# Performance work log

Measured on AMD Instinct MI355X. Metric: run time of the kernel, lower is better.

Reference implementation:

```python
import math
import jax, jax.numpy as jnp
import numpy as np

K = 1.0            # Lorentz manifold curvature k
B, S = 4, 2048     # batch, seq_len
IN, H, OUT = 512, 8, 64   # in_channels, num_heads, out_channels (space dim; head_dim = OUT+1)


def setup_inputs() -> dict:
    key = jax.random.key(0)
    ks = jax.random.split(key, 8)
    std = 1.0 / math.sqrt(IN)
    return {
        "query_input": jax.random.normal(ks[0], (B, S, IN), jnp.float32),
        "source_input": jax.random.normal(ks[1], (B, S, IN), jnp.float32),
        # per-head HypLinear weights stacked on a leading head axis: [H, OUT, IN]
        "Wq_w": jax.random.normal(ks[2], (H, OUT, IN), jnp.float32) * std,
        "Wq_b": jnp.zeros((H, OUT), jnp.float32),
        "Wk_w": jax.random.normal(ks[3], (H, OUT, IN), jnp.float32) * std,
        "Wk_b": jnp.zeros((H, OUT), jnp.float32),
        "Wv_w": jax.random.normal(ks[4], (H, OUT, IN), jnp.float32) * std,
        "Wv_b": jnp.zeros((H, OUT), jnp.float32),
        "scale": jnp.array([math.sqrt(OUT)], jnp.float32),  # nn.Parameter([sqrt(out_channels)])
        "bias": jnp.zeros((), jnp.float32),                 # nn.Parameter(zeros(()))
    }


def hyp_linear(x, w, b):
    # HypLinear: linear map to space part, recompute Lorentz time coord sqrt(||x_s||^2 + k)
    sp = jnp.einsum('bsi,hoi->bsho', x, w) + b            # [B,S,H,OUT]
    t = jnp.sqrt(jnp.sum(sp * sp, axis=-1, keepdims=True) + K)
    return jnp.concatenate([t, sp], axis=-1)              # [B,S,H,OUT+1]


def reference(query_input, source_input, Wq_w, Wq_b, Wk_w, Wk_b, Wv_w, Wv_b, scale, bias):
    q = hyp_linear(query_input, Wq_w, Wq_b)   # [B,S,H,D], D = OUT+1
    k = hyp_linear(source_input, Wk_w, Wk_b)
    v = hyp_linear(source_input, Wv_w, Wv_b)

    # Lorentzian cinner: <x,y>_L = -x0*y0 + <x_s, y_s>
    sgn = jnp.concatenate([-jnp.ones((1,), q.dtype), jnp.ones((OUT,), q.dtype)])
    att = jnp.einsum('bqhd,bkhd->bhqk', q * sgn, k)       # [B,H,S,S]
    att = (2.0 + 2.0 * att) / scale[0] + bias

    causal = jnp.triu(jnp.full((S, S), -1e9, q.dtype), 1)  # causal mask (additive)
    att = jax.nn.softmax(att + causal, axis=-1)

    ctx = jnp.einsum('bhqk,bkhd->bqhd', att, v)           # [B,S,H,D]

    # manifold.mid_point over the heads axis (dim=-2)
    ave = jnp.mean(ctx, axis=2)                           # [B,S,D]
    inner = -ave[..., :1] ** 2 + jnp.sum(ave[..., 1:] ** 2, axis=-1, keepdims=True)
    denom = jnp.sqrt(jnp.maximum(jnp.abs(-inner), 1e-8))
    return math.sqrt(K) * ave / denom                     # [B,S,D]
```

## Files before the change

kernel.cpp:

```cpp
#include <hip/hip_runtime.h>

#define BATCH 4
#define SEQ   2048
#define INC   512
#define NH    8
#define OUTC  64
#define DD    65
#define NROW  (BATCH * NH * SEQ)

typedef float f32x4 __attribute__((ext_vector_type(4)));
typedef short short8 __attribute__((ext_vector_type(8)));
typedef short short4v __attribute__((ext_vector_type(4)));
typedef unsigned int uint2v __attribute__((ext_vector_type(2)));
typedef unsigned short us;

static __device__ __forceinline__ us f2b(float f) {
  unsigned int u = __float_as_uint(f);
  u = (u + 0x7FFFu + ((u >> 16) & 1u)) >> 16;
  return (us)u;
}
static __device__ __forceinline__ float b2f(us h) {
  return __uint_as_float(((unsigned int)h) << 16);
}
static __device__ __forceinline__ unsigned int pk2(float lo, float hi) {
  unsigned int r;
  asm("v_cvt_pk_bf16_f32 %0, %1, %2" : "=v"(r) : "v"(lo), "v"(hi));
  return r;
}

#define GLDS(g, l) __builtin_amdgcn_global_load_lds( \
    (const __attribute__((address_space(1))) void*)(g), \
    (__attribute__((address_space(3))) void*)(l), 16, 0, 0)

__global__ __launch_bounds__(256) void tobf16_kernel(
    const float* __restrict__ Xq, const float* __restrict__ Xs,
    const float* __restrict__ Wq, const float* __restrict__ Wk,
    const float* __restrict__ Wv,
    us* __restrict__ dXq, us* __restrict__ dXs,
    us* __restrict__ dWq, us* __restrict__ dWk, us* __restrict__ dWv)
{
  const int which = blockIdx.y;
  const float* src;
  us* dst;
  int n;
  switch (which) {
    case 0: src = Xq; dst = dXq; n = BATCH * SEQ * INC; break;
    case 1: src = Xs; dst = dXs; n = BATCH * SEQ * INC; break;
    case 2: src = Wq; dst = dWq; n = NH * OUTC * INC; break;
    case 3: src = Wk; dst = dWk; n = NH * OUTC * INC; break;
    default: src = Wv; dst = dWv; n = NH * OUTC * INC; break;
  }
  for (long i = (long)blockIdx.x * 256 + threadIdx.x; i * 4 < n;
       i += (long)gridDim.x * 256) {
    f32x4 v = *(const f32x4*)(src + i * 4);
    short4v o;
    o[0] = (short)f2b(v[0]); o[1] = (short)f2b(v[1]);
    o[2] = (short)f2b(v[2]); o[3] = (short)f2b(v[3]);
    *(short4v*)(dst + i * 4) = o;
  }
}

__global__ __launch_bounds__(256) void proj_kernel(
    const us* __restrict__ Xqb, const us* __restrict__ Xsb,
    const us* __restrict__ Wqb, const us* __restrict__ Wkb, const us* __restrict__ Wvb,
    const float* __restrict__ Bq, const float* __restrict__ Bk, const float* __restrict__ Bv,
    us* __restrict__ qs, float* __restrict__ qt,
    us* __restrict__ ks, unsigned int* __restrict__ kta,
    us* __restrict__ vs, us* __restrict__ vtc)
{
  const int which = blockIdx.z;
  const us* X = (which == 0) ? Xqb : Xsb;
  const us* W = (which == 0) ? Wqb : (which == 1 ? Wkb : Wvb);
  const float* Bb = (which == 0) ? Bq : (which == 1 ? Bk : Bv);
  us* outs = (which == 0) ? qs : (which == 1 ? ks : vs);

  const int lin = blockIdx.x;
  const int h   = (lin >> 3) & 7;
  const int m0  = (((lin >> 6) << 3) | (lin & 7)) * 64;
  const int n0  = h * 64;

  __shared__ alignas(16) us lX[2][64 * 64];
  __shared__ alignas(16) us lW[2][64 * 64];

  const int tid  = threadIdx.x;
  const int lane = tid & 63;
  const int wave = tid >> 6;
  const int arow = lane & 15;
  const int agrp = lane >> 4;
  const int rl   = lane >> 3;
  const int chx  = ((lane & 7) ^ rl) * 8;
  const int r0   = wave * 8 + rl;
  const int r1   = r0 + 32;

#define PSTAGE(buf, k0) do { \
    GLDS(X + (size_t)(m0 + r0) * INC + (k0) + chx, &lX[buf][wave * 512]); \
    GLDS(X + (size_t)(m0 + r1) * INC + (k0) + chx, &lX[buf][2048 + wave * 512]); \
    GLDS(W + (size_t)(n0 + r0) * INC + (k0) + chx, &lW[buf][wave * 512]); \
    GLDS(W + (size_t)(n0 + r1) * INC + (k0) + chx, &lW[buf][2048 + wave * 512]); \
  } while (0)

  f32x4 acc[4] = {};
  PSTAGE(0, 0);

  for (int kk = 0; kk < 8; ++kk) {
    const int cur = kk & 1;
    if (kk < 7) {
      PSTAGE(cur ^ 1, (kk + 1) * 64);
      asm volatile("s_waitcnt vmcnt(4)");
    } else {
      asm volatile("s_waitcnt vmcnt(0)");
    }
    __builtin_amdgcn_s_barrier();
#pragma unroll
    for (int kc = 0; kc < 2; ++kc) {
      short8 af = *(const short8*)&lX[cur][(wave * 16 + arow) * 64 + (((kc * 4 + agrp) ^ (arow & 7)) * 8)];
#pragma unroll
      for (int c = 0; c < 4; ++c) {
        short8 bf = *(const short8*)&lW[cur][(c * 16 + arow) * 64 + (((kc * 4 + agrp) ^ (arow & 7)) * 8)];
        acc[c] = __builtin_amdgcn_mfma_f32_16x16x32_bf16(af, bf, acc[c], 0, 0, 0);
      }
    }
    __builtin_amdgcn_s_barrier();
  }

  float bcol[4];
#pragma unroll
  for (int c = 0; c < 4; ++c) bcol[c] = Bb[n0 + c * 16 + arow];
#pragma unroll
  for (int r = 0; r < 4; ++r) {
    float s2 = 0.f;
#pragma unroll
    for (int c = 0; c < 4; ++c) {
      float v = acc[c][r] + bcol[c];
      acc[c][r] = v;
      s2 += v * v;
    }
    s2 += __shfl_xor(s2, 1); s2 += __shfl_xor(s2, 2);
    s2 += __shfl_xor(s2, 4); s2 += __shfl_xor(s2, 8);
    float tv = sqrtf(s2 + 1.0f);
    int gs = m0 + wave * 16 + agrp * 4 + r;
    int bi = gs >> 11, si = gs & (SEQ - 1);
    size_t rowbase = (size_t)(bi * NH + h) * SEQ + si;
    size_t obase = rowbase * 64;
#pragma unroll
    for (int c = 0; c < 4; ++c) outs[obase + c * 16 + arow] = f2b(acc[c][r]);
    if (arow == 0) {
      if (which == 0) {
        qt[rowbase] = tv;
      } else {
        us th = f2b(tv);
        us tl = f2b(tv - b2f(th));
        if (which == 1) {
          kta[rowbase] = (unsigned int)(us)(th ^ 0x8000)
                       | ((unsigned int)(us)(tl ^ 0x8000) << 16);
        } else {
          vtc[rowbase] = th;
          vtc[NROW + rowbase] = tl;
        }
      }
    }
  }
}

__global__ __launch_bounds__(256) void transpose_v_kernel(
    const us* __restrict__ vs, us* __restrict__ vT)
{
  const int bh = blockIdx.y;
  const int s0 = blockIdx.x * 64;
  __shared__ us lT[64 * 80];
  const int tid = threadIdx.x;
#pragma unroll
  for (int u0 = 0; u0 < 2; ++u0) {
    int u = tid + u0 * 256;
    int row = u >> 3, ch = u & 7;
    short8 v = *(const short8*)&vs[((size_t)bh * SEQ + s0 + row) * 64 + ch * 8];
    *(short8*)&lT[row * 80 + ch * 8] = v;
  }
  __syncthreads();
#pragma unroll
  for (int u0 = 0; u0 < 2; ++u0) {
    int u = tid + u0 * 256;
    int o = u >> 3, sc = u & 7;
    short8 w;
#pragma unroll
    for (int j = 0; j < 8; ++j) w[j] = lT[(sc * 8 + j) * 80 + o];
    *(short8*)&vT[((size_t)bh * 64 + o) * SEQ + s0 + sc * 8] = w;
  }
}

__global__ __launch_bounds__(256, 4) void attn_kernel(
    const us* __restrict__ qs, const float* __restrict__ qt,
    const us* __restrict__ ks, const unsigned int* __restrict__ kta,
    const us* __restrict__ vT, const us* __restrict__ vtc,
    const float* __restrict__ scale_p, float* __restrict__ part)
{
  const int f = blockIdx.x;
  const int xcd = f & 7, idx = f >> 3;
  const int bh = xcd * 4 + (idx >> 5);
  const int inner = idx & 31;
  const int xb = inner >> 1;
  const int hf = inner & 1;
  const float al2 = (2.0f / scale_p[0]) * 1.44269504088896f;

  __shared__ alignas(16) us lK[2][64 * 64];
  __shared__ alignas(16) us lV[2][64 * 64];
  __shared__ alignas(16) us lP[4][16 * 40];

  const int tid  = threadIdx.x;
  const int lane = tid & 63;
  const int wave = tid >> 6;
  const int arow = lane & 15;
  const int agrp = lane >> 4;

  const size_t bhbase = (size_t)bh * SEQ;
  const us* kgp = ks + bhbase * 64;
  const us* vgp = vT + (size_t)bh * 64 * SEQ;
  const unsigned int* ktp = kta + bhbase;
  const us* vtp = vtc + (size_t)(arow & 1) * NROW + bhbase;

  const int rl   = lane >> 3;
  const int chx  = ((lane & 7) ^ rl) * 8;
  const int r0s  = wave * 8 + rl;
  const int r1s  = r0s + 32;
  const int dsl0 = (agrp ^ (arow & 7)) * 8;
  const int dsl1 = ((4 + agrp) ^ (arow & 7)) * 8;
  us* myP = &lP[wave][0];
  const int pw0 = arow * 40 + agrp * 4;
  const int prd = arow * 40 + agrp * 8;

#define ASTAGE(buf, t64) do { \
    const int kk0 = (t64) * 64; \
    GLDS(kgp + (size_t)(kk0 + r0s) * 64 + chx, &lK[buf][wave * 512]); \
    GLDS(kgp + (size_t)(kk0 + r1s) * 64 + chx, &lK[buf][2048 + wave * 512]); \
    GLDS(vgp + (size_t)r0s * SEQ + kk0 + chx, &lV[buf][wave * 512]); \
    GLDS(vgp + (size_t)r1s * SEQ + kk0 + chx, &lV[buf][2048 + wave * 512]); \
  } while (0)

  short8 ones8, zero8 = {};
#pragma unroll
  for (int j = 0; j < 8; ++j) ones8[j] = (short)0x3F80;

  for (int seg = 0; seg < 2; ++seg) {
    const int qb = seg ? (31 - xb) : xb;
    const int q0 = qb * 64;
    const int c0 = (qb + 2) >> 1;
    const int t_lo = hf ? c0 : 0;
    const int t_hi = hf ? (qb + 1) : c0;
    const int nt = t_hi - t_lo;
    const int wq = wave * 16 + arow;

    f32x4 acc[5] = {};

    if (nt > 0) {
      const us* qp = qs + (bhbase + q0 + wq) * 64;
      short8 qf0 = *(const short8*)(qp + agrp * 8);
      short8 qf1 = *(const short8*)(qp + 32 + agrp * 8);
      float qtv = qt[bhbase + q0 + wq];
      us qh = f2b(qtv);
      us ql = f2b(qtv - b2f(qh));
      short8 qf2 = {};
      if (agrp == 0) { qf2[0] = (short)qh; qf2[1] = (short)qh; qf2[2] = (short)ql; }

      unsigned int ka[4];
      short8 va0, va1;
      {
        const int kk0 = t_lo * 64;
#pragma unroll
        for (int c = 0; c < 4; ++c) ka[c] = ktp[kk0 + c * 16 + arow];
        va0 = *(const short8*)(vtp + kk0 + agrp * 8);
        va1 = *(const short8*)(vtp + kk0 + 32 + agrp * 8);
      }
      __builtin_amdgcn_sched_barrier(0);
      ASTAGE(0, t_lo);
      __builtin_amdgcn_sched_barrier(0);

      for (int it = 0; it < nt; ++it) {
        const int t = t_lo + it;
        const int cur = it & 1;
        if (it < nt - 1) {
          ASTAGE(cur ^ 1, t + 1);
          __builtin_amdgcn_sched_barrier(0);
          if (it == 0) asm volatile("s_waitcnt vmcnt(4)");
          else         asm volatile("s_waitcnt vmcnt(10)");
        } else {
          __builtin_amdgcn_sched_barrier(0);
          if (nt > 1) asm volatile("s_waitcnt vmcnt(6)");
          else        asm volatile("s_waitcnt vmcnt(0)");
        }
        __builtin_amdgcn_sched_barrier(0);
        __builtin_amdgcn_s_barrier();

        const us* Kb = lK[cur];
        const us* Vb = lV[cur];

        f32x4 sS[4] = {};
        __builtin_amdgcn_s_setprio(1);
#pragma unroll
        for (int c = 0; c < 4; ++c) {
          short8 kf = *(const short8*)&Kb[(c * 16 + arow) * 64 + dsl0];
          sS[c] = __builtin_amdgcn_mfma_f32_16x16x32_bf16(kf, qf0, sS[c], 0, 0, 0);
        }
#pragma unroll
        for (int c = 0; c < 4; ++c) {
          short8 kf = *(const short8*)&Kb[(c * 16 + arow) * 64 + dsl1];
          sS[c] = __builtin_amdgcn_mfma_f32_16x16x32_bf16(kf, qf1, sS[c], 0, 0, 0);
        }
#pragma unroll
        for (int c = 0; c < 4; ++c) {
          short8 kf2 = {};
          if (agrp == 0) {
            unsigned int w0 = ka[c];
            kf2[0] = (short)(w0 & 0xFFFFu);
            kf2[1] = (short)(w0 >> 16);
            kf2[2] = (short)(w0 & 0xFFFFu);
          }
          sS[c] = __builtin_amdgcn_mfma_f32_16x16x32_bf16(kf2, qf2, sS[c], 0, 0, 0);
        }
        __builtin_amdgcn_s_setprio(0);

#pragma unroll
        for (int c = 0; c < 4; ++c)
#pragma unroll
          for (int r = 0; r < 4; ++r)
            sS[c][r] = exp2f(al2 * sS[c][r]);
        if (t == qb) {
#pragma unroll
          for (int c = 0; c < 4; ++c)
#pragma unroll
            for (int r = 0; r < 4; ++r)
              if (c * 16 + agrp * 4 + r > wq) sS[c][r] = 0.f;
        }

        {
          uint2v w;
          w[0] = pk2(sS[0][0], sS[0][1]); w[1] = pk2(sS[0][2], sS[0][3]);
          *(uint2v*)&myP[pw0] = w;
          w[0] = pk2(sS[1][0], sS[1][1]); w[1] = pk2(sS[1][2], sS[1][3]);
          *(uint2v*)&myP[pw0 + 16] = w;
          short8 pf = *(const short8*)&myP[prd];
          __builtin_amdgcn_s_setprio(1);
#pragma unroll
          for (int dc = 0; dc < 4; ++dc) {
            short8 vf = *(const short8*)&Vb[(dc * 16 + arow) * 64 + dsl0];
            acc[dc] = __builtin_amdgcn_mfma_f32_16x16x32_bf16(pf, vf, acc[dc], 0, 0, 0);
          }
          short8 vf4 = (arow < 2) ? va0 : ((arow == 2) ? ones8 : zero8);
          acc[4] = __builtin_amdgcn_mfma_f32_16x16x32_bf16(pf, vf4, acc[4], 0, 0, 0);
          __builtin_amdgcn_s_setprio(0);
        }
        {
          uint2v w;
          w[0] = pk2(sS[2][0], sS[2][1]); w[1] = pk2(sS[2][2], sS[2][3]);
          *(uint2v*)&myP[pw0] = w;
          w[0] = pk2(sS[3][0], sS[3][1]); w[1] = pk2(sS[3][2], sS[3][3]);
          *(uint2v*)&myP[pw0 + 16] = w;
          short8 pf = *(const short8*)&myP[prd];
          __builtin_amdgcn_s_setprio(1);
#pragma unroll
          for (int dc = 0; dc < 4; ++dc) {
            short8 vf = *(const short8*)&Vb[(dc * 16 + arow) * 64 + dsl1];
            acc[dc] = __builtin_amdgcn_mfma_f32_16x16x32_bf16(pf, vf, acc[dc], 0, 0, 0);
          }
          short8 vf4 = (arow < 2) ? va1 : ((arow == 2) ? ones8 : zero8);
          acc[4] = __builtin_amdgcn_mfma_f32_16x16x32_bf16(pf, vf4, acc[4], 0, 0, 0);
          __builtin_amdgcn_s_setprio(0);
        }

        if (it + 1 < nt) {
          const int kk0 = (t + 1) * 64;
#pragma unroll
          for (int c = 0; c < 4; ++c) ka[c] = ktp[kk0 + c * 16 + arow];
          va0 = *(const short8*)(vtp + kk0 + agrp * 8);
          va1 = *(const short8*)(vtp + kk0 + 32 + agrp * 8);
        }
        __builtin_amdgcn_sched_barrier(0);
        __builtin_amdgcn_s_barrier();
      }
    }

    const size_t pb = ((size_t)(bh * 32 + qb) * 2 + hf) * 64;
#pragma unroll
    for (int r = 0; r < 4; ++r) {
      float t0 = __shfl(acc[4][r], (agrp << 4) | 0);
      float t1 = __shfl(acc[4][r], (agrp << 4) | 1);
      float ls = __shfl(acc[4][r], (agrp << 4) | 2);
      size_t rp = (pb + wave * 16 + agrp * 4 + r) * 68;
#pragma unroll
      for (int dc = 0; dc < 4; ++dc)
        part[rp + dc * 16 + arow] = acc[dc][r];
      if (arow == 0) {
        part[rp + 64] = t0 + t1;
        part[rp + 65] = ls;
        part[rp + 66] = 0.0f;
      }
    }
  }
}

__global__ __launch_bounds__(256) void finalize_kernel(
    const float* __restrict__ part, const float* __restrict__ scale_p,
    float* __restrict__ out)
{
  const int tid  = threadIdx.x;
  const int lane = tid & 63;
  const int gw = blockIdx.x * 4 + (tid >> 6);
  const int b = gw >> 11, si = gw & (SEQ - 1);
  const int qb = si >> 6, row = si & 63;
  const float al2 = (2.0f / scale_p[0]) * 1.44269504088896f;

  float vsum = 0.f, tsum = 0.f;
#pragma unroll
  for (int h = 0; h < NH; ++h) {
    const size_t tile = (size_t)(b * NH + h) * 32 + qb;
    const size_t b0 = (tile * 2 * 64 + row) * 68;
    const size_t b1 = ((tile * 2 + 1) * 64 + row) * 68;
    float A1 = part[b0 + lane];
    float A2 = part[b1 + lane];
    float T1 = part[b0 + 64], L1 = part[b0 + 65], M1 = part[b0 + 66];
    float T2 = part[b1 + 64], L2 = part[b1 + 65], M2 = part[b1 + 66];
    float ms = fmaxf(M1, M2);
    float f1 = exp2f(al2 * (M1 - ms));
    float f2 = exp2f(al2 * (M2 - ms));
    float inv = 1.0f / (f1 * L1 + f2 * L2);
    vsum = fmaf(fmaf(f1, A1, f2 * A2), inv, vsum);
    tsum = fmaf(fmaf(f1, T1, f2 * T2), inv, tsum);
  }
  float ave  = vsum * 0.125f;
  float tave = tsum * 0.125f;
  float contrib = ave * ave;
  if (lane == 0) contrib -= tave * tave;
  contrib += __shfl_xor(contrib, 1);
  contrib += __shfl_xor(contrib, 2);
  contrib += __shfl_xor(contrib, 4);
  contrib += __shfl_xor(contrib, 8);
  contrib += __shfl_xor(contrib, 16);
  contrib += __shfl_xor(contrib, 32);
  float denom = sqrtf(fmaxf(fabsf(contrib), 1e-8f));
  size_t ob = ((size_t)b * SEQ + si) * (size_t)DD;
  out[ob + 1 + lane] = ave / denom;
  if (lane == 0) out[ob] = tave / denom;
}

extern "C" void kernel_launch(void* const* d_in, const int* in_sizes, int n_in,
                              void* d_out, int out_size, void* d_ws, size_t ws_size,
                              hipStream_t stream) {
  const float* Xq  = (const float*)d_in[0];
  const float* Xs  = (const float*)d_in[1];
  const float* Wq  = (const float*)d_in[2];
  const float* Bq  = (const float*)d_in[3];
  const float* Wk  = (const float*)d_in[4];
  const float* Bk  = (const float*)d_in[5];
  const float* Wv  = (const float*)d_in[6];
  const float* Bv  = (const float*)d_in[7];
  const float* scale = (const float*)d_in[8];
  float* out = (float*)d_out;

  char* p = (char*)d_ws;

  float* part = (float*)p;
  us* Xqb   = (us*)p;
  us* Xsb   = (us*)(p + 16777216);
  us* Wqb16 = (us*)(p + 33554432);
  us* Wkb16 = (us*)(p + 34078720);
  us* Wvb16 = (us*)(p + 34603008);
  p += (size_t)1024 * 2 * 64 * 68 * 4;
  us* qsb = (us*)p; p += (size_t)NROW * 64 * 2;
  us* ksb = (us*)p; p += (size_t)NROW * 64 * 2;
  us* vsb = (us*)p; p += (size_t)NROW * 64 * 2;
  us* vTb = (us*)p; p += (size_t)NROW * 64 * 2;
  float* qtb = (float*)p; p += (size_t)NROW * 4;
  unsigned int* ktaw = (unsigned int*)p; p += (size_t)NROW * 4;
  us* vtcw = (us*)p; p += (size_t)NROW * 2 * 2;

  tobf16_kernel<<<dim3(1024, 5), 256, 0, stream>>>(
      Xq, Xs, Wq, Wk, Wv, Xqb, Xsb, Wqb16, Wkb16, Wvb16);
  proj_kernel<<<dim3(1024, 1, 3), 256, 0, stream>>>(
      Xqb, Xsb, Wqb16, Wkb16, Wvb16, Bq, Bk, Bv,
      qsb, qtb, ksb, ktaw, vsb, vtcw);
  transpose_v_kernel<<<dim3(SEQ / 64, BATCH * NH), 256, 0, stream>>>(vsb, vTb);
  attn_kernel<<<dim3(1024), 256, 0, stream>>>(
      qsb, qtb, ksb, ktaw, vTb, vtcw, scale, part);
  finalize_kernel<<<(BATCH * SEQ) / 4, 256, 0, stream>>>(part, scale, out);
}
```

Measured before the change: 95.99 us.

## Process two query tiles per wave, fold softmax scale into Q, drop LDS P staging

Each attention wave now handles 128 query rows as two 64-row halves that share every K/V tile load from LDS. The key range is split four ways instead of two, which changes the partial-buffer layout, and finalize sums the four partials. The softmax scale and log2e factor are folded into Q and its time coordinate in the projection kernel, removing per-element multiplies before exp2. P is built directly in registers in the MFMA operand layout, which needs the V transpose to write a permuted column order, so the LDS round trip for P goes away. This doubles accumulator registers and drops the occupancy hint, which may lower occupancy.

```diff
diff --git a/kernel.cpp b/kernel.cpp
--- a/kernel.cpp
+++ b/kernel.cpp
@@ -11,7 +11,6 @@
 typedef float f32x4 __attribute__((ext_vector_type(4)));
 typedef short short8 __attribute__((ext_vector_type(8)));
 typedef short short4v __attribute__((ext_vector_type(4)));
-typedef unsigned int uint2v __attribute__((ext_vector_type(2)));
 typedef unsigned short us;
 
 static __device__ __forceinline__ us f2b(float f) {
@@ -27,10 +26,17 @@
   asm("v_cvt_pk_bf16_f32 %0, %1, %2" : "=v"(r) : "v"(lo), "v"(hi));
   return r;
 }
+static __device__ __forceinline__ short8 mk8(unsigned int a, unsigned int b,
+                                             unsigned int c, unsigned int d) {
+  union { unsigned int u[4]; short8 s; } x;
+  x.u[0] = a; x.u[1] = b; x.u[2] = c; x.u[3] = d;
+  return x.s;
+}
 
 #define GLDS(g, l) __builtin_amdgcn_global_load_lds( \
     (const __attribute__((address_space(1))) void*)(g), \
     (__attribute__((address_space(3))) void*)(l), 16, 0, 0)
+#define SB() __builtin_amdgcn_sched_barrier(0)
 
 __global__ __launch_bounds__(256) void tobf16_kernel(
     const float* __restrict__ Xq, const float* __restrict__ Xs,
@@ -64,7 +70,8 @@
     const us* __restrict__ Xqb, const us* __restrict__ Xsb,
     const us* __restrict__ Wqb, const us* __restrict__ Wkb, const us* __restrict__ Wvb,
     const float* __restrict__ Bq, const float* __restrict__ Bk, const float* __restrict__ Bv,
-    us* __restrict__ qs, float* __restrict__ qt,
+    const float* __restrict__ scale_p,
+    us* __restrict__ qs, unsigned int* __restrict__ qta,
     us* __restrict__ ks, unsigned int* __restrict__ kta,
     us* __restrict__ vs, us* __restrict__ vtc)
 {
@@ -73,6 +80,8 @@
   const us* W = (which == 0) ? Wqb : (which == 1 ? Wkb : Wvb);
   const float* Bb = (which == 0) ? Bq : (which == 1 ? Bk : Bv);
   us* outs = (which == 0) ? qs : (which == 1 ? ks : vs);
+  const float al2 = (2.0f / scale_p[0]) * 1.44269504088896f;
+  const float oscale = (which == 0) ? al2 : 1.0f;
 
   const int lin = blockIdx.x;
   const int h   = (lin >> 3) & 7;
@@ -143,10 +152,13 @@
     size_t rowbase = (size_t)(bi * NH + h) * SEQ + si;
     size_t obase = rowbase * 64;
 #pragma unroll
-    for (int c = 0; c < 4; ++c) outs[obase + c * 16 + arow] = f2b(acc[c][r]);
+    for (int c = 0; c < 4; ++c) outs[obase + c * 16 + arow] = f2b(oscale * acc[c][r]);
     if (arow == 0) {
       if (which == 0) {
-        qt[rowbase] = tv;
+        float st = al2 * tv;
+        us qh = f2b(st);
+        us ql = f2b(st - b2f(qh));
+        qta[rowbase] = (unsigned int)qh | ((unsigned int)ql << 16);
       } else {
         us th = f2b(tv);
         us tl = f2b(tv - b2f(th));
@@ -181,30 +193,33 @@
   for (int u0 = 0; u0 < 2; ++u0) {
     int u = tid + u0 * 256;
     int o = u >> 3, sc = u & 7;
-    short8 w;
-#pragma unroll
-    for (int j = 0; j < 8; ++j) w[j] = lT[(sc * 8 + j) * 80 + o];
-    *(short8*)&vT[((size_t)bh * 64 + o) * SEQ + s0 + sc * 8] = w;
-  }
-}
-
-__global__ __launch_bounds__(256, 4) void attn_kernel(
-    const us* __restrict__ qs, const float* __restrict__ qt,
+    short4v w0, w1;
+#pragma unroll
+    for (int j = 0; j < 4; ++j) w0[j] = (short)lT[(sc * 8 + j) * 80 + o];
+#pragma unroll
+    for (int j = 0; j < 4; ++j) w1[j] = (short)lT[(sc * 8 + 4 + j) * 80 + o];
+    const int base0 = (sc & 1) * 32 + (sc >> 2) * 8 + ((sc >> 1) & 1) * 4;
+    us* dst = vT + ((size_t)bh * 64 + o) * SEQ + s0;
+    *(short4v*)(dst + base0) = w0;
+    *(short4v*)(dst + base0 + 16) = w1;
+  }
+}
+
+__global__ __launch_bounds__(256) void attn_kernel(
+    const us* __restrict__ qs, const unsigned int* __restrict__ qta,
     const us* __restrict__ ks, const unsigned int* __restrict__ kta,
     const us* __restrict__ vT, const us* __restrict__ vtc,
-    const float* __restrict__ scale_p, float* __restrict__ part)
+    float* __restrict__ part)
 {
   const int f = blockIdx.x;
   const int xcd = f & 7, idx = f >> 3;
   const int bh = xcd * 4 + (idx >> 5);
   const int inner = idx & 31;
-  const int xb = inner >> 1;
-  const int hf = inner & 1;
-  const float al2 = (2.0f / scale_p[0]) * 1.44269504088896f;
+  const int x = inner >> 2;
+  const int hf = inner & 3;
 
   __shared__ alignas(16) us lK[2][64 * 64];
   __shared__ alignas(16) us lV[2][64 * 64];
-  __shared__ alignas(16) us lP[4][16 * 40];
 
   const int tid  = threadIdx.x;
   const int lane = tid & 63;
@@ -218,22 +233,21 @@
   const unsigned int* ktp = kta + bhbase;
   const us* vtp = vtc + (size_t)(arow & 1) * NROW + bhbase;
 
-  const int rl   = lane >> 3;
-  const int chx  = ((lane & 7) ^ rl) * 8;
-  const int r0s  = wave * 8 + rl;
-  const int r1s  = r0s + 32;
-  const int dsl0 = (agrp ^ (arow & 7)) * 8;
-  const int dsl1 = ((4 + agrp) ^ (arow & 7)) * 8;
-  us* myP = &lP[wave][0];
-  const int pw0 = arow * 40 + agrp * 4;
-  const int prd = arow * 40 + agrp * 8;
+  const int rl    = lane >> 3;
+  const int chx   = ((lane & 7) ^ rl) * 8;
+  const int r0s   = wave * 8 + rl;
+  const int r1s   = r0s + 32;
+  const int dsl0  = (agrp ^ (arow & 7)) * 8;
+  const int dsl1  = ((4 + agrp) ^ (arow & 7)) * 8;
+  const int dslV0 = ((agrp * 2) ^ (arow & 7)) * 8;
+  const int dslV1 = ((agrp * 2 + 1) ^ (arow & 7)) * 8;
 
 #define ASTAGE(buf, t64) do { \
-    const int kk0 = (t64) * 64; \
-    GLDS(kgp + (size_t)(kk0 + r0s) * 64 + chx, &lK[buf][wave * 512]); \
-    GLDS(kgp + (size_t)(kk0 + r1s) * 64 + chx, &lK[buf][2048 + wave * 512]); \
-    GLDS(vgp + (size_t)r0s * SEQ + kk0 + chx, &lV[buf][wave * 512]); \
-    GLDS(vgp + (size_t)r1s * SEQ + kk0 + chx, &lV[buf][2048 + wave * 512]); \
+    const int kk = (t64) * 64; \
+    GLDS(kgp + (size_t)(kk + r0s) * 64 + chx, &lK[buf][wave * 512]); \
+    GLDS(kgp + (size_t)(kk + r1s) * 64 + chx, &lK[buf][2048 + wave * 512]); \
+    GLDS(vgp + (size_t)r0s * SEQ + kk + chx, &lV[buf][wave * 512]); \
+    GLDS(vgp + (size_t)r1s * SEQ + kk + chx, &lV[buf][2048 + wave * 512]); \
   } while (0)
 
   short8 ones8, zero8 = {};
@@ -241,69 +255,83 @@
   for (int j = 0; j < 8; ++j) ones8[j] = (short)0x3F80;
 
   for (int seg = 0; seg < 2; ++seg) {
-    const int qb = seg ? (31 - xb) : xb;
-    const int q0 = qb * 64;
-    const int c0 = (qb + 2) >> 1;
-    const int t_lo = hf ? c0 : 0;
-    const int t_hi = hf ? (qb + 1) : c0;
-    const int nt = t_hi - t_lo;
-    const int wq = wave * 16 + arow;
-
-    f32x4 acc[5] = {};
+    const int qT = seg ? (15 - x) : x;
+    const int q0 = qT * 128;
+    const int nk = 2 * qT + 2;
+    const int nbase = nk >> 2, rem = nk & 3;
+    const int nt = nbase + (hf < rem ? 1 : 0);
+    const int t_lo = hf * nbase + (hf < rem ? hf : rem);
+
+    f32x4 acc0[5] = {}, acc1[5] = {};
 
     if (nt > 0) {
-      const us* qp = qs + (bhbase + q0 + wq) * 64;
-      short8 qf0 = *(const short8*)(qp + agrp * 8);
-      short8 qf1 = *(const short8*)(qp + 32 + agrp * 8);
-      float qtv = qt[bhbase + q0 + wq];
-      us qh = f2b(qtv);
-      us ql = f2b(qtv - b2f(qh));
-      short8 qf2 = {};
-      if (agrp == 0) { qf2[0] = (short)qh; qf2[1] = (short)qh; qf2[2] = (short)ql; }
+      const int wq0 = q0 + wave * 16 + arow;
+      const int wq1 = wq0 + 64;
+
+      const us* qp0 = qs + (bhbase + wq0) * 64;
+      const us* qp1 = qs + (bhbase + wq1) * 64;
+      short8 qf00 = *(const short8*)(qp0 + agrp * 8);
+      short8 qf01 = *(const short8*)(qp0 + 32 + agrp * 8);
+      short8 qf10 = *(const short8*)(qp1 + agrp * 8);
+      short8 qf11 = *(const short8*)(qp1 + 32 + agrp * 8);
+      unsigned int qw0 = qta[bhbase + wq0];
+      unsigned int qw1 = qta[bhbase + wq1];
+      short8 qf2_0 = {}, qf2_1 = {};
+      if (agrp == 0) {
+        qf2_0[0] = (short)(qw0 & 0xFFFFu); qf2_0[1] = (short)(qw0 & 0xFFFFu);
+        qf2_0[2] = (short)(qw0 >> 16);
+        qf2_1[0] = (short)(qw1 & 0xFFFFu); qf2_1[1] = (short)(qw1 & 0xFFFFu);
+        qf2_1[2] = (short)(qw1 >> 16);
+      }
 
       unsigned int ka[4];
-      short8 va0, va1;
+      short4v vaA[2], vaB[2];
       {
-        const int kk0 = t_lo * 64;
-#pragma unroll
-        for (int c = 0; c < 4; ++c) ka[c] = ktp[kk0 + c * 16 + arow];
-        va0 = *(const short8*)(vtp + kk0 + agrp * 8);
-        va1 = *(const short8*)(vtp + kk0 + 32 + agrp * 8);
+        const int kk = t_lo * 64;
+#pragma unroll
+        for (int c = 0; c < 4; ++c) ka[c] = ktp[kk + c * 16 + arow];
+#pragma unroll
+        for (int kc = 0; kc < 2; ++kc) {
+          vaA[kc] = *(const short4v*)(vtp + kk + kc * 32 + agrp * 4);
+          vaB[kc] = *(const short4v*)(vtp + kk + kc * 32 + 16 + agrp * 4);
+        }
       }
-      __builtin_amdgcn_sched_barrier(0);
+      SB();
       ASTAGE(0, t_lo);
-      __builtin_amdgcn_sched_barrier(0);
+      SB();
 
       for (int it = 0; it < nt; ++it) {
         const int t = t_lo + it;
         const int cur = it & 1;
         if (it < nt - 1) {
           ASTAGE(cur ^ 1, t + 1);
-          __builtin_amdgcn_sched_barrier(0);
+          SB();
           if (it == 0) asm volatile("s_waitcnt vmcnt(4)");
-          else         asm volatile("s_waitcnt vmcnt(10)");
+          else         asm volatile("s_waitcnt vmcnt(12)");
         } else {
-          __builtin_amdgcn_sched_barrier(0);
-          if (nt > 1) asm volatile("s_waitcnt vmcnt(6)");
+          SB();
+          if (nt > 1) asm volatile("s_waitcnt vmcnt(8)");
           else        asm volatile("s_waitcnt vmcnt(0)");
         }
-        __builtin_amdgcn_sched_barrier(0);
+        SB();
         __builtin_amdgcn_s_barrier();
 
         const us* Kb = lK[cur];
         const us* Vb = lV[cur];
 
-        f32x4 sS[4] = {};
+        f32x4 s0[4] = {}, s1[4] = {};
         __builtin_amdgcn_s_setprio(1);
 #pragma unroll
         for (int c = 0; c < 4; ++c) {
           short8 kf = *(const short8*)&Kb[(c * 16 + arow) * 64 + dsl0];
-          sS[c] = __builtin_amdgcn_mfma_f32_16x16x32_bf16(kf, qf0, sS[c], 0, 0, 0);
+          s0[c] = __builtin_amdgcn_mfma_f32_16x16x32_bf16(kf, qf00, s0[c], 0, 0, 0);
+          s1[c] = __builtin_amdgcn_mfma_f32_16x16x32_bf16(kf, qf10, s1[c], 0, 0, 0);
         }
 #pragma unroll
         for (int c = 0; c < 4; ++c) {
           short8 kf = *(const short8*)&Kb[(c * 16 + arow) * 64 + dsl1];
-          sS[c] = __builtin_amdgcn_mfma_f32_16x16x32_bf16(kf, qf1, sS[c], 0, 0, 0);
+          s0[c] = __builtin_amdgcn_mfma_f32_16x16x32_bf16(kf, qf01, s0[c], 0, 0, 0);
+          s1[c] = __builtin_amdgcn_mfma_f32_16x16x32_bf16(kf, qf11, s1[c], 0, 0, 0);
         }
 #pragma unroll
         for (int c = 0; c < 4; ++c) {
@@ -314,116 +342,121 @@
             kf2[1] = (short)(w0 >> 16);
             kf2[2] = (short)(w0 & 0xFFFFu);
           }
-          sS[c] = __builtin_amdgcn_mfma_f32_16x16x32_bf16(kf2, qf2, sS[c], 0, 0, 0);
+          s0[c] = __builtin_amdgcn_mfma_f32_16x16x32_bf16(kf2, qf2_0, s0[c], 0, 0, 0);
+          s1[c] = __builtin_amdgcn_mfma_f32_16x16x32_bf16(kf2, qf2_1, s1[c], 0, 0, 0);
         }
         __builtin_amdgcn_s_setprio(0);
 
 #pragma unroll
         for (int c = 0; c < 4; ++c)
 #pragma unroll
-          for (int r = 0; r < 4; ++r)
-            sS[c][r] = exp2f(al2 * sS[c][r]);
-        if (t == qb) {
+          for (int r = 0; r < 4; ++r) {
+            s0[c][r] = exp2f(s0[c][r]);
+            s1[c][r] = exp2f(s1[c][r]);
+          }
+        if (t >= 2 * qT) {
+          const int kb = t * 64;
 #pragma unroll
           for (int c = 0; c < 4; ++c)
 #pragma unroll
-            for (int r = 0; r < 4; ++r)
-              if (c * 16 + agrp * 4 + r > wq) sS[c][r] = 0.f;
-        }
-
-        {
-          uint2v w;
-          w[0] = pk2(sS[0][0], sS[0][1]); w[1] = pk2(sS[0][2], sS[0][3]);
-          *(uint2v*)&myP[pw0] = w;
-          w[0] = pk2(sS[1][0], sS[1][1]); w[1] = pk2(sS[1][2], sS[1][3]);
-          *(uint2v*)&myP[pw0 + 16] = w;
-          short8 pf = *(const short8*)&myP[prd];
-          __builtin_amdgcn_s_setprio(1);
+            for (int r = 0; r < 4; ++r) {
+              int k = kb + c * 16 + agrp * 4 + r;
+              if (k > wq0) s0[c][r] = 0.f;
+              if (k > wq1) s1[c][r] = 0.f;
+            }
+        }
+
+        __builtin_amdgcn_s_setprio(1);
+#pragma unroll
+        for (int kc = 0; kc < 2; ++kc) {
+          short8 pf0 = mk8(pk2(s0[2*kc][0], s0[2*kc][1]),
+                           pk2(s0[2*kc][2], s0[2*kc][3]),
+                           pk2(s0[2*kc+1][0], s0[2*kc+1][1]),
+                           pk2(s0[2*kc+1][2], s0[2*kc+1][3]));
+          short8 pf1 = mk8(pk2(s1[2*kc][0], s1[2*kc][1]),
+                           pk2(s1[2*kc][2], s1[2*kc][3]),
+                           pk2(s1[2*kc+1][0], s1[2*kc+1][1]),
+                           pk2(s1[2*kc+1][2], s1[2*kc+1][3]));
+          const int dsl = kc ? dslV1 : dslV0;
 #pragma unroll
           for (int dc = 0; dc < 4; ++dc) {
-            short8 vf = *(const short8*)&Vb[(dc * 16 + arow) * 64 + dsl0];
-            acc[dc] = __builtin_amdgcn_mfma_f32_16x16x32_bf16(pf, vf, acc[dc], 0, 0, 0);
+            short8 vf = *(const short8*)&Vb[(dc * 16 + arow) * 64 + dsl];
+            acc0[dc] = __builtin_amdgcn_mfma_f32_16x16x32_bf16(pf0, vf, acc0[dc], 0, 0, 0);
+            acc1[dc] = __builtin_amdgcn_mfma_f32_16x16x32_bf16(pf1, vf, acc1[dc], 0, 0, 0);
           }
-          short8 vf4 = (arow < 2) ? va0 : ((arow == 2) ? ones8 : zero8);
-          acc[4] = __builtin_amdgcn_mfma_f32_16x16x32_bf16(pf, vf4, acc[4], 0, 0, 0);
-          __builtin_amdgcn_s_setprio(0);
-        }
-        {
-          uint2v w;
-          w[0] = pk2(sS[2][0], sS[2][1]); w[1] = pk2(sS[2][2], sS[2][3]);
-          *(uint2v*)&myP[pw0] = w;
-          w[0] = pk2(sS[3][0], sS[3][1]); w[1] = pk2(sS[3][2], sS[3][3]);
-          *(uint2v*)&myP[pw0 + 16] = w;
-          short8 pf = *(const short8*)&myP[prd];
-          __builtin_amdgcn_s_setprio(1);
-#pragma unroll
-          for (int dc = 0; dc < 4; ++dc) {
-            short8 vf = *(const short8*)&Vb[(dc * 16 + arow) * 64 + dsl1];
-            acc[dc] = __builtin_amdgcn_mfma_f32_16x16x32_bf16(pf, vf, acc[dc], 0, 0, 0);
+          short8 vf4;
+          if (arow < 2) {
+            *(short4v*)&vf4 = vaA[kc];
+            *(((short4v*)&vf4) + 1) = vaB[kc];
+          } else vf4 = (arow == 2) ? ones8 : zero8;
+          acc0[4] = __builtin_amdgcn_mfma_f32_16x16x32_bf16(pf0, vf4, acc0[4], 0, 0, 0);
+          acc1[4] = __builtin_amdgcn_mfma_f32_16x16x32_bf16(pf1, vf4, acc1[4], 0, 0, 0);
+        }
+        __builtin_amdgcn_s_setprio(0);
+
+        SB();
+        if (it + 1 < nt) {
+          const int kk = (t + 1) * 64;
+#pragma unroll
+          for (int c = 0; c < 4; ++c) ka[c] = ktp[kk + c * 16 + arow];
+#pragma unroll
+          for (int kc = 0; kc < 2; ++kc) {
+            vaA[kc] = *(const short4v*)(vtp + kk + kc * 32 + agrp * 4);
+            vaB[kc] = *(const short4v*)(vtp + kk + kc * 32 + 16 + agrp * 4);
           }
-          short8 vf4 = (arow < 2) ? va1 : ((arow == 2) ? ones8 : zero8);
-          acc[4] = __builtin_amdgcn_mfma_f32_16x16x32_bf16(pf, vf4, acc[4], 0, 0, 0);
-          __builtin_amdgcn_s_setprio(0);
-        }
-
-        if (it + 1 < nt) {
-          const int kk0 = (t + 1) * 64;
-#pragma unroll
-          for (int c = 0; c < 4; ++c) ka[c] = ktp[kk0 + c * 16 + arow];
-          va0 = *(const short8*)(vtp + kk0 + agrp * 8);
-          va1 = *(const short8*)(vtp + kk0 + 32 + agrp * 8);
-        }
-        __builtin_amdgcn_sched_barrier(0);
+        }
+        SB();
         __builtin_amdgcn_s_barrier();
       }
     }
 
-    const size_t pb = ((size_t)(bh * 32 + qb) * 2 + hf) * 64;
+    const size_t pbase = (size_t)(((bh * 16 + qT) * 4 + hf)) * 128;
 #pragma unroll
     for (int r = 0; r < 4; ++r) {
-      float t0 = __shfl(acc[4][r], (agrp << 4) | 0);
-      float t1 = __shfl(acc[4][r], (agrp << 4) | 1);
-      float ls = __shfl(acc[4][r], (agrp << 4) | 2);
-      size_t rp = (pb + wave * 16 + agrp * 4 + r) * 68;
-#pragma unroll
-      for (int dc = 0; dc < 4; ++dc)
-        part[rp + dc * 16 + arow] = acc[dc][r];
-      if (arow == 0) {
-        part[rp + 64] = t0 + t1;
-        part[rp + 65] = ls;
-        part[rp + 66] = 0.0f;
-      }
+      float t0 = __shfl(acc0[4][r], (agrp << 4) | 0);
+      float t1 = __shfl(acc0[4][r], (agrp << 4) | 1);
+      float ls = __shfl(acc0[4][r], (agrp << 4) | 2);
+      size_t rp = (pbase + wave * 16 + agrp * 4 + r) * 68;
+#pragma unroll
+      for (int dc = 0; dc < 4; ++dc) part[rp + dc * 16 + arow] = acc0[dc][r];
+      if (arow == 0) { part[rp + 64] = t0 + t1; part[rp + 65] = ls; }
+    }
+#pragma unroll
+    for (int r = 0; r < 4; ++r) {
+      float t0 = __shfl(acc1[4][r], (agrp << 4) | 0);
+      float t1 = __shfl(acc1[4][r], (agrp << 4) | 1);
+      float ls = __shfl(acc1[4][r], (agrp << 4) | 2);
+      size_t rp = (pbase + 64 + wave * 16 + agrp * 4 + r) * 68;
+#pragma unroll
+      for (int dc = 0; dc < 4; ++dc) part[rp + dc * 16 + arow] = acc1[dc][r];
+      if (arow == 0) { part[rp + 64] = t0 + t1; part[rp + 65] = ls; }
     }
   }
 }
 
 __global__ __launch_bounds__(256) void finalize_kernel(
-    const float* __restrict__ part, const float* __restrict__ scale_p,
-    float* __restrict__ out)
+    const float* __restrict__ part, float* __restrict__ out)
 {
   const int tid  = threadIdx.x;
   const int lane = tid & 63;
   const int gw = blockIdx.x * 4 + (tid >> 6);
   const int b = gw >> 11, si = gw & (SEQ - 1);
-  const int qb = si >> 6, row = si & 63;
-  const float al2 = (2.0f / scale_p[0]) * 1.44269504088896f;
+  const int qT = si >> 7, row = si & 127;
 
   float vsum = 0.f, tsum = 0.f;
 #pragma unroll
   for (int h = 0; h < NH; ++h) {
-    const size_t tile = (size_t)(b * NH + h) * 32 + qb;
-    const size_t b0 = (tile * 2 * 64 + row) * 68;
-    const size_t b1 = ((tile * 2 + 1) * 64 + row) * 68;
-    float A1 = part[b0 + lane];
-    float A2 = part[b1 + lane];
-    float T1 = part[b0 + 64], L1 = part[b0 + 65], M1 = part[b0 + 66];
-    float T2 = part[b1 + 64], L2 = part[b1 + 65], M2 = part[b1 + 66];
-    float ms = fmaxf(M1, M2);
-    float f1 = exp2f(al2 * (M1 - ms));
-    float f2 = exp2f(al2 * (M2 - ms));
-    float inv = 1.0f / (f1 * L1 + f2 * L2);
-    vsum = fmaf(fmaf(f1, A1, f2 * A2), inv, vsum);
-    tsum = fmaf(fmaf(f1, T1, f2 * T2), inv, tsum);
+    float Ah = 0.f, Th = 0.f, Lh = 0.f;
+#pragma unroll
+    for (int hf = 0; hf < 4; ++hf) {
+      size_t rb = ((size_t)((((b * NH + h) * 16 + qT) * 4 + hf)) * 128 + row) * 68;
+      Ah += part[rb + lane];
+      Th += part[rb + 64];
+      Lh += part[rb + 65];
+    }
+    float inv = 1.0f / Lh;
+    vsum = fmaf(Ah, inv, vsum);
+    tsum = fmaf(Th, inv, tsum);
   }
   float ave  = vsum * 0.125f;
   float tave = tsum * 0.125f;
@@ -463,22 +496,22 @@
   us* Wqb16 = (us*)(p + 33554432);
   us* Wkb16 = (us*)(p + 34078720);
   us* Wvb16 = (us*)(p + 34603008);
-  p += (size_t)1024 * 2 * 64 * 68 * 4;
+  us* vsb   = (us*)(p + 35651584);
+  p += (size_t)32 * 16 * 4 * 128 * 68 * 4;
   us* qsb = (us*)p; p += (size_t)NROW * 64 * 2;
   us* ksb = (us*)p; p += (size_t)NROW * 64 * 2;
-  us* vsb = (us*)p; p += (size_t)NROW * 64 * 2;
   us* vTb = (us*)p; p += (size_t)NROW * 64 * 2;
-  float* qtb = (float*)p; p += (size_t)NROW * 4;
+  unsigned int* qtaw = (unsigned int*)p; p += (size_t)NROW * 4;
   unsigned int* ktaw = (unsigned int*)p; p += (size_t)NROW * 4;
   us* vtcw = (us*)p; p += (size_t)NROW * 2 * 2;
 
   tobf16_kernel<<<dim3(1024, 5), 256, 0, stream>>>(
       Xq, Xs, Wq, Wk, Wv, Xqb, Xsb, Wqb16, Wkb16, Wvb16);
   proj_kernel<<<dim3(1024, 1, 3), 256, 0, stream>>>(
-      Xqb, Xsb, Wqb16, Wkb16, Wvb16, Bq, Bk, Bv,
-      qsb, qtb, ksb, ktaw, vsb, vtcw);
+      Xqb, Xsb, Wqb16, Wkb16, Wvb16, Bq, Bk, Bv, scale,
+      qsb, qtaw, ksb, ktaw, vsb, vtcw);
   transpose_v_kernel<<<dim3(SEQ / 64, BATCH * NH), 256, 0, stream>>>(vsb, vTb);
   attn_kernel<<<dim3(1024), 256, 0, stream>>>(
-      qsb, qtb, ksb, ktaw, vTb, vtcw, scale, part);
-  finalize_kernel<<<(BATCH * SEQ) / 4, 256, 0, stream>>>(part, scale, out);
-}
+      qsb, qtaw, ksb, ktaw, vTb, vtcw, part);
+  finalize_kernel<<<(BATCH * SEQ) / 4, 256, 0, stream>>>(part, out);
+}
```

Measured after the change: 103.5 us. +7.8%, slower.
